# Performance work log

Hardware: AMD Instinct MI355X
Metric: run time of the kernel (lower is better)

The kernel has to match this reference:

```python
import jax, jax.numpy as jnp
import numpy as np


def setup_inputs() -> dict:
    key = jax.random.key(0)
    k1, k2, k3, k4 = jax.random.split(key, 4)
    in_f, out_f, rank, tokens = 4096, 4096, 256, 8192
    bound = 1.0 / np.sqrt(in_f)
    x = jax.random.normal(k1, (tokens, in_f), dtype=jnp.float32)
    U = jax.random.uniform(k2, (out_f, rank), dtype=jnp.float32, minval=-bound, maxval=bound)
    V = jax.random.uniform(k3, (rank, in_f), dtype=jnp.float32, minval=-bound, maxval=bound)
    bias = jax.random.uniform(k4, (out_f,), dtype=jnp.float32, minval=-bound, maxval=bound)
    return {"x": x, "U": U, "V": V, "bias": bias}


def reference(x, U, V, bias):
    # Faithful to original: materialize W = U @ V, then F.linear(x, W, bias) = x @ W.T + bias
    W = U @ V                      # [out, in]
    return x @ W.T + bias          # [tokens, out]
```

## Files before the change

kernel.cpp:

```cpp
#include <hip/hip_runtime.h>
#include <stdint.h>

#define TOKENS 8192
#define INF    4096
#define OUTF   4096
#define RANK   256

typedef __attribute__((ext_vector_type(8))) short bf16x8;
typedef __attribute__((ext_vector_type(4))) float f32x4;

__device__ __forceinline__ unsigned short f2bf(float f) {
    union { float f; unsigned int u; } v; v.f = f;
    unsigned int r = v.u + 0x7FFFu + ((v.u >> 16) & 1u);
    return (unsigned short)(r >> 16);
}

__device__ __forceinline__ void gl_lds16(const void* g, void* l) {
    __builtin_amdgcn_global_load_lds(
        (const __attribute__((address_space(1))) unsigned int*)g,
        (__attribute__((address_space(3))) unsigned int*)l, 16, 0, 0);
}

__global__ void cvt4(const float4* __restrict__ in, ushort4* __restrict__ out) {
    int i = blockIdx.x * blockDim.x + threadIdx.x;
    float4 v = in[i];
    ushort4 o;
    o.x = f2bf(v.x); o.y = f2bf(v.y); o.z = f2bf(v.z); o.w = f2bf(v.w);
    out[i] = o;
}

#define G1_BM 32
#define G1_BK 64
#define A1_STRIDE 72

__global__ __launch_bounds__(256) void gemm1(const float* __restrict__ x,
                                             const unsigned short* __restrict__ Vb,
                                             unsigned short* __restrict__ T) {
    __shared__ __align__(16) unsigned short Alds[G1_BM * A1_STRIDE];
    __shared__ __align__(16) unsigned short Blds[RANK * G1_BK];

    const int tid  = threadIdx.x;
    const int lane = tid & 63;
    const int wid  = tid >> 6;
    const int m0   = blockIdx.x * G1_BM;
    const int l15  = lane & 15;
    const int quad = lane >> 4;

    const int arow = tid >> 3;
    const int aseg = tid & 7;
    const float* xa = x + (size_t)(m0 + arow) * INF + aseg * 8;
    unsigned short* alds_w = &Alds[arow * A1_STRIDE + aseg * 8];

    const int b_lrow = lane >> 3;
    const int b_cf   = (lane & 7) ^ b_lrow;

    f32x4 acc[2][4];
    #pragma unroll
    for (int i = 0; i < 2; i++)
        #pragma unroll
        for (int j = 0; j < 4; j++) acc[i][j] = (f32x4){0.f, 0.f, 0.f, 0.f};

    for (int kk = 0; kk < INF; kk += G1_BK) {
        #pragma unroll
        for (int j = 0; j < 8; ++j) {
            int r0 = wid * 64 + j * 8;
            gl_lds16(Vb + (size_t)(r0 + b_lrow) * INF + kk + b_cf * 8,
                     &Blds[r0 * G1_BK]);
        }
        float4 va = *(const float4*)(xa + kk);
        float4 vb = *(const float4*)(xa + kk + 4);
        {
            union { bf16x8 v; unsigned short s[8]; } pk;
            pk.s[0] = f2bf(va.x); pk.s[1] = f2bf(va.y);
            pk.s[2] = f2bf(va.z); pk.s[3] = f2bf(va.w);
            pk.s[4] = f2bf(vb.x); pk.s[5] = f2bf(vb.y);
            pk.s[6] = f2bf(vb.z); pk.s[7] = f2bf(vb.w);
            *(bf16x8*)alds_w = pk.v;
        }
        __syncthreads();
        #pragma unroll
        for (int ks = 0; ks < 2; ++ks) {
            bf16x8 af[2], bfr[4];
            #pragma unroll
            for (int mt = 0; mt < 2; ++mt) {
                int row = mt * 16 + l15;
                af[mt] = *(const bf16x8*)&Alds[row * A1_STRIDE + ks * 32 + quad * 8];
            }
            #pragma unroll
            for (int nt = 0; nt < 4; ++nt) {
                int n   = wid * 64 + nt * 16 + l15;
                int pos = (ks * 4 + quad) ^ (l15 & 7);
                bfr[nt] = *(const bf16x8*)&Blds[n * G1_BK + pos * 8];
            }
            #pragma unroll
            for (int mt = 0; mt < 2; ++mt)
                #pragma unroll
                for (int nt = 0; nt < 4; ++nt)
                    acc[mt][nt] = __builtin_amdgcn_mfma_f32_16x16x32_bf16(
                        af[mt], bfr[nt], acc[mt][nt], 0, 0, 0);
        }
        __syncthreads();
    }
    #pragma unroll
    for (int mt = 0; mt < 2; ++mt)
        #pragma unroll
        for (int nt = 0; nt < 4; ++nt) {
            int col = wid * 64 + nt * 16 + l15;
            #pragma unroll
            for (int r = 0; r < 4; ++r) {
                int row = m0 + mt * 16 + quad * 4 + r;
                T[(size_t)row * RANK + col] = f2bf(acc[mt][nt][r]);
            }
        }
}

#define G2_BM 128
#define G2_BN 128
#define G2_BK 64

__global__ __launch_bounds__(256) void gemm2(const unsigned short* __restrict__ Tb,
                                             const unsigned short* __restrict__ Ub,
                                             const float* __restrict__ bias,
                                             float* __restrict__ out) {
    __shared__ __align__(16) unsigned short Alds[G2_BM * G2_BK];
    __shared__ __align__(16) unsigned short Blds[G2_BN * G2_BK];

    const int tid  = threadIdx.x;
    const int lane = tid & 63;
    const int wid  = tid >> 6;
    const int wy   = wid >> 1, wx = wid & 1;
    const int m0   = blockIdx.y * G2_BM;
    const int n0   = blockIdx.x * G2_BN;
    const int l15  = lane & 15, quad = lane >> 4;
    const int lrow = lane >> 3;
    const int cf   = (lane & 7) ^ lrow;

    f32x4 acc[4][4];
    #pragma unroll
    for (int i = 0; i < 4; i++)
        #pragma unroll
        for (int j = 0; j < 4; j++) acc[i][j] = (f32x4){0.f, 0.f, 0.f, 0.f};

    for (int kk = 0; kk < RANK; kk += G2_BK) {
        #pragma unroll
        for (int j = 0; j < 4; ++j) {
            int r0 = wid * 32 + j * 8;
            gl_lds16(Tb + (size_t)(m0 + r0 + lrow) * RANK + kk + cf * 8,
                     &Alds[r0 * G2_BK]);
            gl_lds16(Ub + (size_t)(n0 + r0 + lrow) * RANK + kk + cf * 8,
                     &Blds[r0 * G2_BK]);
        }
        __syncthreads();
        #pragma unroll
        for (int ks = 0; ks < 2; ++ks) {
            bf16x8 af[4], bfr[4];
            #pragma unroll
            for (int t = 0; t < 4; ++t) {
                int ar = wy * 64 + t * 16 + l15;
                int ap = (ks * 4 + quad) ^ (ar & 7);
                af[t] = *(const bf16x8*)&Alds[ar * G2_BK + ap * 8];
                int br = wx * 64 + t * 16 + l15;
                int bp = (ks * 4 + quad) ^ (br & 7);
                bfr[t] = *(const bf16x8*)&Blds[br * G2_BK + bp * 8];
            }
            #pragma unroll
            for (int mt = 0; mt < 4; ++mt)
                #pragma unroll
                for (int nt = 0; nt < 4; ++nt)
                    acc[mt][nt] = __builtin_amdgcn_mfma_f32_16x16x32_bf16(
                        af[mt], bfr[nt], acc[mt][nt], 0, 0, 0);
        }
        __syncthreads();
    }
    float bv[4];
    #pragma unroll
    for (int nt = 0; nt < 4; ++nt) bv[nt] = bias[n0 + wx * 64 + nt * 16 + l15];
    #pragma unroll
    for (int mt = 0; mt < 4; ++mt)
        #pragma unroll
        for (int nt = 0; nt < 4; ++nt) {
            int col = n0 + wx * 64 + nt * 16 + l15;
            #pragma unroll
            for (int r = 0; r < 4; ++r) {
                int row = m0 + wy * 64 + mt * 16 + quad * 4 + r;
                out[(size_t)row * OUTF + col] = acc[mt][nt][r] + bv[nt];
            }
        }
}

extern "C" void kernel_launch(void* const* d_in, const int* in_sizes, int n_in,
                              void* d_out, int out_size, void* d_ws, size_t ws_size,
                              hipStream_t stream) {
    const float* x    = (const float*)d_in[0];
    const float* U    = (const float*)d_in[1];
    const float* V    = (const float*)d_in[2];
    const float* bias = (const float*)d_in[3];
    float* out = (float*)d_out;

    unsigned short* Vb = (unsigned short*)d_ws;
    unsigned short* Ub = Vb + (size_t)RANK * INF;
    unsigned short* Tb = Ub + (size_t)OUTF * RANK;

    cvt4<<<(RANK * INF / 4) / 256, 256, 0, stream>>>((const float4*)V, (ushort4*)Vb);
    cvt4<<<(OUTF * RANK / 4) / 256, 256, 0, stream>>>((const float4*)U, (ushort4*)Ub);
    gemm1<<<TOKENS / G1_BM, 256, 0, stream>>>(x, Vb, Tb);
    gemm2<<<dim3(OUTF / G2_BN, TOKENS / G2_BM), 256, 0, stream>>>(Tb, Ub, bias, out);
}
```

Baseline: 303.8 us.

## Swap MFMA operand roles for vectorized stores and retile first GEMM over rank

The first GEMM now tiles the rank dimension across two blocks, using 512 threads and a K-step of 128. It computes the transposed product so that each lane holds four consecutive columns and can write them as one ushort4. The second GEMM likewise swaps operands (U as A, T as B), so outputs are written as float4 with a vectorized bias load instead of scalar strided stores. The goal is to cut non-coalesced epilogue traffic and raise parallelism in the first GEMM. The cost is that x is now read and converted twice, once per rank half.

```diff
diff --git a/kernel.cpp b/kernel.cpp
--- a/kernel.cpp
+++ b/kernel.cpp
@@ -30,42 +30,44 @@
 }
 
 #define G1_BM 32
-#define G1_BK 64
-#define A1_STRIDE 72
-
-__global__ __launch_bounds__(256) void gemm1(const float* __restrict__ x,
+#define G1_BN 128
+#define G1_BK 128
+#define A1_STR 136
+
+__global__ __launch_bounds__(512) void gemm1(const float* __restrict__ x,
                                              const unsigned short* __restrict__ Vb,
                                              unsigned short* __restrict__ T) {
-    __shared__ __align__(16) unsigned short Alds[G1_BM * A1_STRIDE];
-    __shared__ __align__(16) unsigned short Blds[RANK * G1_BK];
+    __shared__ __align__(16) unsigned short Axlds[G1_BM * A1_STR];
+    __shared__ __align__(16) unsigned short Bvlds[G1_BN * G1_BK];
 
     const int tid  = threadIdx.x;
     const int lane = tid & 63;
     const int wid  = tid >> 6;
-    const int m0   = blockIdx.x * G1_BM;
+    const int m0   = blockIdx.y * G1_BM;
+    const int n0   = blockIdx.x * G1_BN;
     const int l15  = lane & 15;
     const int quad = lane >> 4;
 
-    const int arow = tid >> 3;
-    const int aseg = tid & 7;
+    const int arow = tid >> 4;
+    const int aseg = tid & 15;
     const float* xa = x + (size_t)(m0 + arow) * INF + aseg * 8;
-    unsigned short* alds_w = &Alds[arow * A1_STRIDE + aseg * 8];
-
-    const int b_lrow = lane >> 3;
-    const int b_cf   = (lane & 7) ^ b_lrow;
-
-    f32x4 acc[2][4];
-    #pragma unroll
-    for (int i = 0; i < 2; i++)
-        #pragma unroll
-        for (int j = 0; j < 4; j++) acc[i][j] = (f32x4){0.f, 0.f, 0.f, 0.f};
+    unsigned short* alds_w = &Axlds[arow * A1_STR + aseg * 8];
+
+    const int b_lrow = lane >> 4;
+    const int b_pos  = lane & 15;
+
+    f32x4 acc[2];
+    acc[0] = (f32x4){0.f, 0.f, 0.f, 0.f};
+    acc[1] = (f32x4){0.f, 0.f, 0.f, 0.f};
 
     for (int kk = 0; kk < INF; kk += G1_BK) {
         #pragma unroll
-        for (int j = 0; j < 8; ++j) {
-            int r0 = wid * 64 + j * 8;
-            gl_lds16(Vb + (size_t)(r0 + b_lrow) * INF + kk + b_cf * 8,
-                     &Blds[r0 * G1_BK]);
+        for (int j = 0; j < 4; ++j) {
+            int r0  = j * 32 + wid * 4;
+            int row = r0 + b_lrow;
+            int cf  = b_pos ^ (row & 7);
+            gl_lds16(Vb + (size_t)(n0 + row) * INF + kk + cf * 8,
+                     &Bvlds[r0 * G1_BK]);
         }
         float4 va = *(const float4*)(xa + kk);
         float4 vb = *(const float4*)(xa + kk + 4);
@@ -79,39 +81,28 @@
         }
         __syncthreads();
         #pragma unroll
-        for (int ks = 0; ks < 2; ++ks) {
-            bf16x8 af[2], bfr[4];
+        for (int ks = 0; ks < 4; ++ks) {
+            int rr = wid * 16 + l15;
+            int p  = (ks * 4 + quad) ^ (rr & 7);
+            bf16x8 aV = *(const bf16x8*)&Bvlds[rr * G1_BK + p * 8];
             #pragma unroll
             for (int mt = 0; mt < 2; ++mt) {
-                int row = mt * 16 + l15;
-                af[mt] = *(const bf16x8*)&Alds[row * A1_STRIDE + ks * 32 + quad * 8];
+                int tr = mt * 16 + l15;
+                bf16x8 bx = *(const bf16x8*)&Axlds[tr * A1_STR + ks * 32 + quad * 8];
+                acc[mt] = __builtin_amdgcn_mfma_f32_16x16x32_bf16(aV, bx, acc[mt], 0, 0, 0);
             }
-            #pragma unroll
-            for (int nt = 0; nt < 4; ++nt) {
-                int n   = wid * 64 + nt * 16 + l15;
-                int pos = (ks * 4 + quad) ^ (l15 & 7);
-                bfr[nt] = *(const bf16x8*)&Blds[n * G1_BK + pos * 8];
-            }
-            #pragma unroll
-            for (int mt = 0; mt < 2; ++mt)
-                #pragma unroll
-                for (int nt = 0; nt < 4; ++nt)
-                    acc[mt][nt] = __builtin_amdgcn_mfma_f32_16x16x32_bf16(
-                        af[mt], bfr[nt], acc[mt][nt], 0, 0, 0);
-        }
-        __syncthreads();
-    }
-    #pragma unroll
-    for (int mt = 0; mt < 2; ++mt)
-        #pragma unroll
-        for (int nt = 0; nt < 4; ++nt) {
-            int col = wid * 64 + nt * 16 + l15;
-            #pragma unroll
-            for (int r = 0; r < 4; ++r) {
-                int row = m0 + mt * 16 + quad * 4 + r;
-                T[(size_t)row * RANK + col] = f2bf(acc[mt][nt][r]);
-            }
-        }
+        }
+        __syncthreads();
+    }
+    #pragma unroll
+    for (int mt = 0; mt < 2; ++mt) {
+        int m      = m0 + mt * 16 + l15;
+        int n_base = n0 + wid * 16 + quad * 4;
+        ushort4 o;
+        o.x = f2bf(acc[mt][0]); o.y = f2bf(acc[mt][1]);
+        o.z = f2bf(acc[mt][2]); o.w = f2bf(acc[mt][3]);
+        *(ushort4*)&T[(size_t)m * RANK + n_base] = o;
+    }
 }
 
 #define G2_BM 128
@@ -122,8 +113,8 @@
                                              const unsigned short* __restrict__ Ub,
                                              const float* __restrict__ bias,
                                              float* __restrict__ out) {
-    __shared__ __align__(16) unsigned short Alds[G2_BM * G2_BK];
-    __shared__ __align__(16) unsigned short Blds[G2_BN * G2_BK];
+    __shared__ __align__(16) unsigned short Tlds[G2_BM * G2_BK];
+    __shared__ __align__(16) unsigned short Ulds[G2_BN * G2_BK];
 
     const int tid  = threadIdx.x;
     const int lane = tid & 63;
@@ -146,46 +137,50 @@
         for (int j = 0; j < 4; ++j) {
             int r0 = wid * 32 + j * 8;
             gl_lds16(Tb + (size_t)(m0 + r0 + lrow) * RANK + kk + cf * 8,
-                     &Alds[r0 * G2_BK]);
+                     &Tlds[r0 * G2_BK]);
             gl_lds16(Ub + (size_t)(n0 + r0 + lrow) * RANK + kk + cf * 8,
-                     &Blds[r0 * G2_BK]);
+                     &Ulds[r0 * G2_BK]);
         }
         __syncthreads();
         #pragma unroll
         for (int ks = 0; ks < 2; ++ks) {
-            bf16x8 af[4], bfr[4];
+            bf16x8 aU[4], bT[4];
             #pragma unroll
             for (int t = 0; t < 4; ++t) {
-                int ar = wy * 64 + t * 16 + l15;
-                int ap = (ks * 4 + quad) ^ (ar & 7);
-                af[t] = *(const bf16x8*)&Alds[ar * G2_BK + ap * 8];
-                int br = wx * 64 + t * 16 + l15;
-                int bp = (ks * 4 + quad) ^ (br & 7);
-                bfr[t] = *(const bf16x8*)&Blds[br * G2_BK + bp * 8];
+                int ur = wx * 64 + t * 16 + l15;
+                int up = (ks * 4 + quad) ^ (ur & 7);
+                aU[t] = *(const bf16x8*)&Ulds[ur * G2_BK + up * 8];
+                int tr = wy * 64 + t * 16 + l15;
+                int tp = (ks * 4 + quad) ^ (tr & 7);
+                bT[t] = *(const bf16x8*)&Tlds[tr * G2_BK + tp * 8];
             }
             #pragma unroll
-            for (int mt = 0; mt < 4; ++mt)
+            for (int nt = 0; nt < 4; ++nt)
                 #pragma unroll
-                for (int nt = 0; nt < 4; ++nt)
-                    acc[mt][nt] = __builtin_amdgcn_mfma_f32_16x16x32_bf16(
-                        af[mt], bfr[nt], acc[mt][nt], 0, 0, 0);
-        }
-        __syncthreads();
-    }
-    float bv[4];
-    #pragma unroll
-    for (int nt = 0; nt < 4; ++nt) bv[nt] = bias[n0 + wx * 64 + nt * 16 + l15];
-    #pragma unroll
-    for (int mt = 0; mt < 4; ++mt)
-        #pragma unroll
-        for (int nt = 0; nt < 4; ++nt) {
-            int col = n0 + wx * 64 + nt * 16 + l15;
-            #pragma unroll
-            for (int r = 0; r < 4; ++r) {
-                int row = m0 + wy * 64 + mt * 16 + quad * 4 + r;
-                out[(size_t)row * OUTF + col] = acc[mt][nt][r] + bv[nt];
-            }
-        }
+                for (int mt = 0; mt < 4; ++mt)
+                    acc[nt][mt] = __builtin_amdgcn_mfma_f32_16x16x32_bf16(
+                        aU[nt], bT[mt], acc[nt][mt], 0, 0, 0);
+        }
+        __syncthreads();
+    }
+    float4 bv[4];
+    #pragma unroll
+    for (int nt = 0; nt < 4; ++nt)
+        bv[nt] = *(const float4*)&bias[n0 + wx * 64 + nt * 16 + quad * 4];
+    #pragma unroll
+    for (int nt = 0; nt < 4; ++nt) {
+        int n_base = n0 + wx * 64 + nt * 16 + quad * 4;
+        #pragma unroll
+        for (int mt = 0; mt < 4; ++mt) {
+            int m = m0 + wy * 64 + mt * 16 + l15;
+            float4 v;
+            v.x = acc[nt][mt][0] + bv[nt].x;
+            v.y = acc[nt][mt][1] + bv[nt].y;
+            v.z = acc[nt][mt][2] + bv[nt].z;
+            v.w = acc[nt][mt][3] + bv[nt].w;
+            *(float4*)&out[(size_t)m * OUTF + n_base] = v;
+        }
+    }
 }
 
 extern "C" void kernel_launch(void* const* d_in, const int* in_sizes, int n_in,
@@ -203,6 +198,6 @@
 
     cvt4<<<(RANK * INF / 4) / 256, 256, 0, stream>>>((const float4*)V, (ushort4*)Vb);
     cvt4<<<(OUTF * RANK / 4) / 256, 256, 0, stream>>>((const float4*)U, (ushort4*)Ub);
-    gemm1<<<TOKENS / G1_BM, 256, 0, stream>>>(x, Vb, Tb);
+    gemm1<<<dim3(RANK / G1_BN, TOKENS / G1_BM), 512, 0, stream>>>(x, Vb, Tb);
     gemm2<<<dim3(OUTF / G2_BN, TOKENS / G2_BM), 256, 0, stream>>>(Tb, Ub, bias, out);
 }
```

Measured after the change: 293.7 us. -3.3%, faster.
